# Optimization experiments

Measured on AMD Instinct MI355X. Metric: run time of the kernel, lower is better.

Reference implementation:

```python
import jax, jax.numpy as jnp
import numpy as np

D_STATE = 16; D_MODEL = 256; N_HEADS = 8; N_LAYERS = 4; D_REL = 64
HEALTH = 0
WORLD = (1024.0, 1024.0)
B, T, N = 32, 512, 8
ACTION_DIM = 12


def setup_inputs() -> dict:
    key = jax.random.key(0)
    ks = iter(jax.random.split(key, 48))
    s = 0.02
    def w(shape):
        return jax.random.normal(next(ks), shape, jnp.float32) * s
    inp = dict(
        state=jax.random.normal(next(ks), (B, T, N, D_STATE), jnp.float32),
        pos=jax.random.uniform(next(ks), (B, T, N, 2), jnp.float32),
        vel=jax.random.normal(next(ks), (B, T, N, 2), jnp.float32),
        team_ids=jax.random.randint(next(ks), (B, T, N), 0, 2, jnp.int32),
        alive=jax.random.randint(next(ks), (B, T, N), 0, 2, jnp.int32).astype(bool),
        dead=jnp.zeros((D_STATE,), jnp.float32),
        enc_W1=w((D_STATE, D_MODEL)), enc_b1=jnp.zeros((D_MODEL,), jnp.float32),
        enc_W2=w((D_MODEL, D_MODEL)), enc_b2=jnp.zeros((D_MODEL,), jnp.float32),
        team_emb=w((2, D_MODEL)), ship_emb=w((8, D_MODEL)),
        trunk_W1=w((6, D_REL)), trunk_b1=jnp.zeros((D_REL,), jnp.float32),
        trunk_W2=w((D_REL, D_REL)), trunk_b2=jnp.zeros((D_REL,), jnp.float32),
        adapt_W=w((N_LAYERS, D_REL, N_HEADS)), adapt_b=jnp.zeros((N_LAYERS, N_HEADS), jnp.float32),
        norm_w=jnp.ones((N_LAYERS, D_MODEL), jnp.float32),
        Wq=w((N_LAYERS, D_MODEL, D_MODEL)), bq=jnp.zeros((N_LAYERS, D_MODEL), jnp.float32),
        Wk=w((N_LAYERS, D_MODEL, D_MODEL)), bk=jnp.zeros((N_LAYERS, D_MODEL), jnp.float32),
        Wv=w((N_LAYERS, D_MODEL, D_MODEL)), bv=jnp.zeros((N_LAYERS, D_MODEL), jnp.float32),
        Wo=w((N_LAYERS, D_MODEL, D_MODEL)), bo=jnp.zeros((N_LAYERS, D_MODEL), jnp.float32),
        head_W=w((D_MODEL, ACTION_DIM)), head_b=jnp.zeros((ACTION_DIM,), jnp.float32),
    )
    return inp


def _rms(x, g, eps=1e-6):
    return x * jax.lax.rsqrt(jnp.mean(x * x, axis=-1, keepdims=True) + eps) * g


def reference(state, pos, vel, team_ids, alive, dead,
              enc_W1, enc_b1, enc_W2, enc_b2, team_emb, ship_emb,
              trunk_W1, trunk_b1, trunk_W2, trunk_b2, adapt_W, adapt_b,
              norm_w, Wq, bq, Wk, bk, Wv, bv, Wo, bo, head_W, head_b):
    ws = jnp.asarray(WORLD, state.dtype)
    # replace dead entities' state with learned 'dead' vector
    state = jnp.where(alive[..., None], state, dead)
    # state encoder (MLP)
    h = jax.nn.silu(state @ enc_W1 + enc_b1) @ enc_W2 + enc_b2
    # special embeddings
    h = h + team_emb[team_ids] + ship_emb[jnp.arange(N)]  # ship_emb broadcasts over B,T
    # relational trunk: pairwise toroidal geometry features [B,T,N,N,6]
    p = pos * ws
    rel = p[:, :, :, None, :] - p[:, :, None, :, :]
    rel = rel - jnp.round(rel / ws) * ws  # toroidal wrap
    relv = vel[:, :, :, None, :] - vel[:, :, None, :, :]
    dn = jnp.sqrt(jnp.sum(rel * rel, axis=-1) + 1e-8) / ws[0]
    feats = jnp.concatenate([rel / ws, relv, dn[..., None], 1.0 / (1.0 + dn[..., None])], axis=-1)
    trunk = jax.nn.silu(feats @ trunk_W1 + trunk_b1) @ trunk_W2 + trunk_b2  # [B,T,N,N,D_REL]
    dh = D_MODEL // N_HEADS
    scale = dh ** -0.5
    kmask = alive[:, :, None, None, :]  # mask keys
    x = h
    for i in range(N_LAYERS):
        nx = _rms(x, norm_w[i])
        # adapter: per-layer relational bias [B,T,H,N,N]
        bias = jnp.transpose(trunk @ adapt_W[i] + adapt_b[i], (0, 1, 4, 2, 3))
        q = (nx @ Wq[i] + bq[i]).reshape(B, T, N, N_HEADS, dh)
        k = (nx @ Wk[i] + bk[i]).reshape(B, T, N, N_HEADS, dh)
        v = (nx @ Wv[i] + bv[i]).reshape(B, T, N, N_HEADS, dh)
        sc = jnp.einsum('btihd,btjhd->bthij', q, k) * scale + bias
        sc = jnp.where(kmask, sc, -1e9)
        a = jax.nn.softmax(sc, axis=-1)
        o = jnp.einsum('bthij,btjhd->btihd', a, v).reshape(B, T, N, D_MODEL)
        x = x + o @ Wo[i] + bo[i]
    action_logits = x @ head_W + head_b  # [B,T,N,12]
    return action_logits
```

## Files before the change

### kernel.cpp

```cpp
#include <hip/hip_runtime.h>
#include <cstdint>

#define DEV __device__ __forceinline__

typedef __attribute__((ext_vector_type(8))) short short8;
typedef __attribute__((ext_vector_type(4))) float floatx4;
typedef unsigned short u16;

DEV u16 f2bf(float f) {
    unsigned u = __float_as_uint(f);
    return (u16)((u + 0x7fffu + ((u >> 16) & 1u)) >> 16);
}
DEV void unpack2(unsigned u, float& a, float& b) {
    a = __uint_as_float(u << 16);
    b = __uint_as_float(u & 0xffff0000u);
}
DEV void unpack8u(uint4 u, float* f) {
    unpack2(u.x, f[0], f[1]); unpack2(u.y, f[2], f[3]);
    unpack2(u.z, f[4], f[5]); unpack2(u.w, f[6], f[7]);
}
DEV unsigned pack2f(float a, float b) { return (unsigned)f2bf(a) | ((unsigned)f2bf(b) << 16); }
DEV uint4 pack8f(const float* f) {
    uint4 u;
    u.x = pack2f(f[0], f[1]); u.y = pack2f(f[2], f[3]);
    u.z = pack2f(f[4], f[5]); u.w = pack2f(f[6], f[7]);
    return u;
}
DEV float sigm(float x) { return 1.0f / (1.0f + __expf(-x)); }

#define NAG 8
#define DM 256
#define NL 4
#define AD 12
#define TPB 4
#define MROWS 32
#define NBLK 4096

#define OFF_E1   0
#define OFF_E2   8192
#define OFF_QKVO 73728
#define OFF_TW2  1122304
#define OFF_ADW  1126400
#define WS_TOTAL 1128448
#define WS_BYTES (WS_TOTAL * 2)

#define L_R1    0
#define L_R1B   18432
#define L_R2    36864
#define L_RED   53760
#define L_SPOS  54272
#define L_SVEL  54528
#define L_ALV   54784
#define L_TEAM  54912
#define SMEM_BYTES 55040

enum { I_STATE=0, I_POS, I_VEL, I_TEAM, I_ALIVE, I_DEAD, I_EW1, I_EB1, I_EW2, I_EB2,
       I_TEMB, I_SEMB, I_TW1, I_TB1, I_TW2, I_TB2, I_ADW, I_ADB, I_NORMW,
       I_WQ, I_BQ, I_WK, I_BK, I_WV, I_BV, I_WO, I_BO, I_HW, I_HB, N_IN };

struct Args { const void* in[N_IN]; float* out; };

__global__ __launch_bounds__(256) void prep_kernel(Args a, u16* ws)
{
    int e = blockIdx.x * 256 + threadIdx.x;
    int mat = blockIdx.y;
    int size, offs, N, Kreal;
    const float* src;
    if (mat == 0)      { size = 8192;  offs = OFF_E1;  N = 256; Kreal = 16;  src = (const float*)a.in[I_EW1]; }
    else if (mat == 1) { size = 65536; offs = OFF_E2;  N = 256; Kreal = 256; src = (const float*)a.in[I_EW2]; }
    else if (mat < 18) {
        int q = mat - 2, l = q >> 2, m = q & 3;
        int wi = (m == 0) ? I_WQ : (m == 1) ? I_WK : (m == 2) ? I_WV : I_WO;
        size = 65536; offs = OFF_QKVO + q * 65536; N = 256; Kreal = 256;
        src = (const float*)a.in[wi] + l * 65536;
    }
    else if (mat == 18) { size = 4096; offs = OFF_TW2; N = 64; Kreal = 64; src = (const float*)a.in[I_TW2]; }
    else                { size = 2048; offs = OFF_ADW; N = 32; Kreal = 64; src = (const float*)a.in[I_ADW]; }
    if (e >= size) return;
    int ksblk = N * 32;
    int ks = e / ksblk, rem = e % ksblk;
    int n = rem >> 5, quad = (rem >> 3) & 3, j = rem & 7;
    int k = ks * 32 + quad * 8 + j;
    float v = 0.0f;
    if (k < Kreal) {
        if (mat == 19) v = src[((n >> 3) * 64 + k) * 8 + (n & 7)];
        else           v = src[k * N + n];
    }
    ws[offs + e] = f2bf(v);
}

DEV short8 ld_u4(const u16* p) {
    union { uint4 u; short8 s; } c;
    c.u = *(const uint4*)p;
    return c.s;
}
DEV short8 ld_afrag(const u16* A, int stride, int row0, int kofs, int l15, int quad) {
    return ld_u4(A + (row0 + l15) * stride + kofs + quad * 8);
}
DEV short8 ld_bws(const u16* w, int ksblk, int ks, int col, int l15, int quad) {
    return ld_u4(w + ks * ksblk + (col + l15) * 32 + quad * 8);
}
DEV short8 ld_bf32(const float* W, int N, int Kreal, int ks, int col, int l15, int quad) {
    short8 r;
    #pragma unroll
    for (int j = 0; j < 8; j++) {
        int k = ks * 32 + quad * 8 + j;
        float v = (k < Kreal) ? W[k * N + col + l15] : 0.0f;
        r[j] = (short)f2bf(v);
    }
    return r;
}

template<bool UW>
DEV void gemm32(const u16* A, const u16* wsW, const float* Wf,
                int Kb, int Kreal, int colw, int l15, int quad, floatx4 acc[2][4]) {
    for (int ks = 0; ks < Kb; ks++) {
        short8 af0 = ld_afrag(A, 264, 0,  ks * 32, l15, quad);
        short8 af1 = ld_afrag(A, 264, 16, ks * 32, l15, quad);
        short8 bf[4];
        #pragma unroll
        for (int nj = 0; nj < 4; nj++)
            bf[nj] = UW ? ld_bws(wsW, 8192, ks, colw + nj * 16, l15, quad)
                        : ld_bf32(Wf, 256, Kreal, ks, colw + nj * 16, l15, quad);
        #pragma unroll
        for (int nj = 0; nj < 4; nj++) {
            acc[0][nj] = __builtin_amdgcn_mfma_f32_16x16x32_bf16(af0, bf[nj], acc[0][nj], 0, 0, 0);
            acc[1][nj] = __builtin_amdgcn_mfma_f32_16x16x32_bf16(af1, bf[nj], acc[1][nj], 0, 0, 0);
        }
    }
}

template<bool UW>
__global__ __launch_bounds__(256, 2) void yemong_mfma(Args a, const u16* ws)
{
    extern __shared__ char smem[];
    u16* sR1   = (u16*)(smem + L_R1);
    u16* sR1b  = (u16*)(smem + L_R1B);
    u16* sR2   = (u16*)(smem + L_R2);
    float* sred = (float*)(smem + L_RED);
    float* spos = (float*)(smem + L_SPOS);
    float* svel = (float*)(smem + L_SVEL);
    int* salive = (int*)(smem + L_ALV);
    int* steam  = (int*)(smem + L_TEAM);

    const int t = threadIdx.x;
    const int bid = blockIdx.x;
    const int lane = t & 63, wv = t >> 6;
    const int l15 = lane & 15, quad = lane >> 4;
    const int colw = wv * 64;

    float xr[2][4][4];
    float bias_f[4][8];
    const int tok = t >> 6, hh = (t >> 3) & 7, ii = t & 7;

    unsigned mp = 0;
    const unsigned* au = (const unsigned*)a.in[I_ALIVE];
    #pragma unroll
    for (int i = 0; i < 16; i++) mp |= au[i];
    const bool abyte = (mp > 1u);
    auto aliveAt = [&](int r) -> int {
        int gi = bid * MROWS + r;
        return abyte ? (int)((const unsigned char*)a.in[I_ALIVE])[gi]
                     : ((const int*)a.in[I_ALIVE])[gi];
    };

    if (t < MROWS) {
        salive[t] = aliveAt(t) ? 1 : 0;
        steam[t]  = ((const int*)a.in[I_TEAM])[bid * MROWS + t];
    }
    if (t >= 64 && t < 128) {
        int idx = t - 64, n = idx >> 1, d = idx & 1;
        spos[n * 2 + d] = ((const float*)a.in[I_POS])[(bid * MROWS + n) * 2 + d] * 1024.0f;
        svel[n * 2 + d] = ((const float*)a.in[I_VEL])[(bid * MROWS + n) * 2 + d];
    }
    {
        const float* gs = (const float*)a.in[I_STATE];
        const float* gd = (const float*)a.in[I_DEAD];
        #pragma unroll
        for (int it = 0; it < 4; it++) {
            int idx = t + 256 * it;
            int r = idx >> 5, kk = idx & 31;
            float v = 0.0f;
            if (kk < 16) v = aliveAt(r) ? gs[(bid * MROWS + r) * 16 + kk] : gd[kk];
            sR2[r * 264 + kk] = f2bf(v);
        }
    }
    __syncthreads();

    {
        floatx4 acc[2][4] = {};
        gemm32<UW>(sR2, ws + OFF_E1, (const float*)a.in[I_EW1], 1, 16, colw, l15, quad, acc);
        __syncthreads();
        const float* b1 = (const float*)a.in[I_EB1];
        #pragma unroll
        for (int nj = 0; nj < 4; nj++) {
            int c = colw + nj * 16 + l15;
            float bb = b1[c];
            #pragma unroll
            for (int mi = 0; mi < 2; mi++)
                #pragma unroll
                for (int r = 0; r < 4; r++) {
                    int row = mi * 16 + quad * 4 + r;
                    float v = acc[mi][nj][r] + bb;
                    sR2[row * 264 + c] = f2bf(v * sigm(v));
                }
        }
    }
    __syncthreads();

    {
        floatx4 acc[2][4] = {};
        gemm32<UW>(sR2, ws + OFF_E2, (const float*)a.in[I_EW2], 8, 256, colw, l15, quad, acc);
        const float* b2 = (const float*)a.in[I_EB2];
        const float* te = (const float*)a.in[I_TEMB];
        const float* se = (const float*)a.in[I_SEMB];
        #pragma unroll
        for (int nj = 0; nj < 4; nj++) {
            int c = colw + nj * 16 + l15;
            float bb = b2[c];
            #pragma unroll
            for (int mi = 0; mi < 2; mi++)
                #pragma unroll
                for (int r = 0; r < 4; r++) {
                    int row = mi * 16 + quad * 4 + r;
                    xr[mi][nj][r] = acc[mi][nj][r] + bb + te[steam[row] * 256 + c] + se[(row & 7) * 256 + c];
                }
        }
    }
    __syncthreads();

    {
        int ri = tok * 8 + ii, rj = tok * 8 + (t & 7);
        int pi = tok * 8 + ((t >> 3) & 7), pj = tok * 8 + (t & 7);
        float rx = spos[pi * 2 + 0] - spos[pj * 2 + 0];
        float ry = spos[pi * 2 + 1] - spos[pj * 2 + 1];
        rx -= rintf(rx * (1.0f / 1024.0f)) * 1024.0f;
        ry -= rintf(ry * (1.0f / 1024.0f)) * 1024.0f;
        float vx = svel[pi * 2 + 0] - svel[pj * 2 + 0];
        float vy = svel[pi * 2 + 1] - svel[pj * 2 + 1];
        float dn = sqrtf(rx * rx + ry * ry + 1e-8f) * (1.0f / 1024.0f);
        float f0 = rx * (1.0f / 1024.0f), f1 = ry * (1.0f / 1024.0f);
        float f4 = dn, f5 = 1.0f / (1.0f + dn);
        const float* W1 = (const float*)a.in[I_TW1];
        const float* B1 = (const float*)a.in[I_TB1];
        #pragma unroll
        for (int r = 0; r < 64; r += 2) {
            float v0 = B1[r], v1 = B1[r + 1];
            v0 = fmaf(f0, W1[r],       v0); v1 = fmaf(f0, W1[r + 1],       v1);
            v0 = fmaf(f1, W1[64 + r],  v0); v1 = fmaf(f1, W1[64 + r + 1],  v1);
            v0 = fmaf(vx, W1[128 + r], v0); v1 = fmaf(vx, W1[128 + r + 1], v1);
            v0 = fmaf(vy, W1[192 + r], v0); v1 = fmaf(vy, W1[192 + r + 1], v1);
            v0 = fmaf(f4, W1[256 + r], v0); v1 = fmaf(f4, W1[256 + r + 1], v1);
            v0 = fmaf(f5, W1[320 + r], v0); v1 = fmaf(f5, W1[320 + r + 1], v1);
            *(unsigned*)&sR1[t * 72 + r] = pack2f(v0 * sigm(v0), v1 * sigm(v1));
        }
        (void)ri; (void)rj;
    }
    __syncthreads();

    {
        short8 taf[4][2];
        #pragma unroll
        for (int mi = 0; mi < 4; mi++)
            #pragma unroll
            for (int ks = 0; ks < 2; ks++)
                taf[mi][ks] = ld_afrag(sR1, 72, colw + mi * 16, ks * 32, l15, quad);
        floatx4 tacc[4][4] = {};
        #pragma unroll
        for (int ks = 0; ks < 2; ks++) {
            short8 bf[4];
            #pragma unroll
            for (int nj = 0; nj < 4; nj++)
                bf[nj] = UW ? ld_bws(ws + OFF_TW2, 2048, ks, nj * 16, l15, quad)
                            : ld_bf32((const float*)a.in[I_TW2], 64, 64, ks, nj * 16, l15, quad);
            #pragma unroll
            for (int mi = 0; mi < 4; mi++)
                #pragma unroll
                for (int nj = 0; nj < 4; nj++)
                    tacc[mi][nj] = __builtin_amdgcn_mfma_f32_16x16x32_bf16(taf[mi][ks], bf[nj], tacc[mi][nj], 0, 0, 0);
        }
        const float* B2 = (const float*)a.in[I_TB2];
        #pragma unroll
        for (int nj = 0; nj < 4; nj++) {
            int c = nj * 16 + l15;
            float bb = B2[c];
            #pragma unroll
            for (int mi = 0; mi < 4; mi++)
                #pragma unroll
                for (int r = 0; r < 4; r++) {
                    int row = colw + mi * 16 + quad * 4 + r;
                    sR1[row * 72 + c] = f2bf(tacc[mi][nj][r] + bb);
                }
        }
    }
    __syncthreads();

    {
        floatx4 tacc[4][2] = {};
        #pragma unroll
        for (int ks = 0; ks < 2; ks++) {
            short8 bf[2];
            #pragma unroll
            for (int nj = 0; nj < 2; nj++) {
                if (UW) bf[nj] = ld_bws(ws + OFF_ADW, 1024, ks, nj * 16, l15, quad);
                else {
                    const float* adw = (const float*)a.in[I_ADW];
                    int n = nj * 16 + l15;
                    #pragma unroll
                    for (int j = 0; j < 8; j++) {
                        int k = ks * 32 + quad * 8 + j;
                        bf[nj][j] = (short)f2bf(k < 64 ? adw[((n >> 3) * 64 + k) * 8 + (n & 7)] : 0.0f);
                    }
                }
            }
            #pragma unroll
            for (int mi = 0; mi < 4; mi++) {
                short8 af = ld_afrag(sR1, 72, colw + mi * 16, ks * 32, l15, quad);
                #pragma unroll
                for (int nj = 0; nj < 2; nj++)
                    tacc[mi][nj] = __builtin_amdgcn_mfma_f32_16x16x32_bf16(af, bf[nj], tacc[mi][nj], 0, 0, 0);
            }
        }
        const float* adb = (const float*)a.in[I_ADB];
        #pragma unroll
        for (int nj = 0; nj < 2; nj++) {
            int n = nj * 16 + l15;
            float bb = adb[n];
            #pragma unroll
            for (int mi = 0; mi < 4; mi++)
                #pragma unroll
                for (int r = 0; r < 4; r++) {
                    int pl = mi * 16 + quad * 4 + r;
                    sR2[((wv * 4 + (n >> 3)) * 8 + (n & 7)) * 64 + pl] = f2bf(tacc[mi][nj][r] + bb);
                }
        }
        __syncthreads();
        #pragma unroll
        for (int l = 0; l < 4; l++) {
            uint4 u = *(const uint4*)&sR2[((tok * 4 + l) * 8 + hh) * 64 + ii * 8];
            unpack8u(u, bias_f[l]);
        }
    }

    const float* normw = (const float*)a.in[I_NORMW];
    for (int l = 0; l < NL; l++) {
        float invr[8];
        {
            float ssv[8];
            #pragma unroll
            for (int mi = 0; mi < 2; mi++)
                #pragma unroll
                for (int r = 0; r < 4; r++) {
                    float s = 0.0f;
                    #pragma unroll
                    for (int nj = 0; nj < 4; nj++) { float v = xr[mi][nj][r]; s = fmaf(v, v, s); }
                    ssv[mi * 4 + r] = s;
                }
            #pragma unroll
            for (int m = 1; m < 16; m <<= 1)
                #pragma unroll
                for (int k2 = 0; k2 < 8; k2++) ssv[k2] += __shfl_xor(ssv[k2], m);
            if (l15 == 0) {
                #pragma unroll
                for (int mi = 0; mi < 2; mi++)
                    #pragma unroll
                    for (int r = 0; r < 4; r++)
                        sred[(mi * 16 + quad * 4 + r) * 4 + wv] = ssv[mi * 4 + r];
            }
            __syncthreads();
            #pragma unroll
            for (int mi = 0; mi < 2; mi++)
                #pragma unroll
                for (int r = 0; r < 4; r++) {
                    int row = mi * 16 + quad * 4 + r;
                    float s = sred[row * 4 + 0] + sred[row * 4 + 1] + sred[row * 4 + 2] + sred[row * 4 + 3];
                    invr[mi * 4 + r] = rsqrtf(s * (1.0f / 256.0f) + 1e-6f);
                }
        }
        {
            float nwv[4];
            #pragma unroll
            for (int nj = 0; nj < 4; nj++) nwv[nj] = normw[l * 256 + colw + nj * 16 + l15];
            #pragma unroll
            for (int nj = 0; nj < 4; nj++) {
                int c = colw + nj * 16 + l15;
                #pragma unroll
                for (int mi = 0; mi < 2; mi++)
                    #pragma unroll
                    for (int r = 0; r < 4; r++)
                        sR2[(mi * 16 + quad * 4 + r) * 264 + c] = f2bf(xr[mi][nj][r] * invr[mi * 4 + r] * nwv[nj]);
            }
        }
        __syncthreads();

        {
            floatx4 acc[3][2][4] = {};
            const u16* wq = ws + OFF_QKVO + (l * 4 + 0) * 65536;
            const u16* wk = ws + OFF_QKVO + (l * 4 + 1) * 65536;
            const u16* wvv = ws + OFF_QKVO + (l * 4 + 2) * 65536;
            const float* fq = (const float*)a.in[I_WQ] + l * 65536;
            const float* fk = (const float*)a.in[I_WK] + l * 65536;
            const float* fv = (const float*)a.in[I_WV] + l * 65536;
            #pragma unroll 2
            for (int ks = 0; ks < 8; ks++) {
                short8 af0 = ld_afrag(sR2, 264, 0,  ks * 32, l15, quad);
                short8 af1 = ld_afrag(sR2, 264, 16, ks * 32, l15, quad);
                short8 bq[4], bk[4], bv[4];
                #pragma unroll
                for (int nj = 0; nj < 4; nj++) {
                    int c = colw + nj * 16;
                    bq[nj] = UW ? ld_bws(wq,  8192, ks, c, l15, quad) : ld_bf32(fq, 256, 256, ks, c, l15, quad);
                    bk[nj] = UW ? ld_bws(wk,  8192, ks, c, l15, quad) : ld_bf32(fk, 256, 256, ks, c, l15, quad);
                    bv[nj] = UW ? ld_bws(wvv, 8192, ks, c, l15, quad) : ld_bf32(fv, 256, 256, ks, c, l15, quad);
                }
                #pragma unroll
                for (int nj = 0; nj < 4; nj++) {
                    acc[0][0][nj] = __builtin_amdgcn_mfma_f32_16x16x32_bf16(af0, bq[nj], acc[0][0][nj], 0, 0, 0);
                    acc[0][1][nj] = __builtin_amdgcn_mfma_f32_16x16x32_bf16(af1, bq[nj], acc[0][1][nj], 0, 0, 0);
                    acc[1][0][nj] = __builtin_amdgcn_mfma_f32_16x16x32_bf16(af0, bk[nj], acc[1][0][nj], 0, 0, 0);
                    acc[1][1][nj] = __builtin_amdgcn_mfma_f32_16x16x32_bf16(af1, bk[nj], acc[1][1][nj], 0, 0, 0);
                    acc[2][0][nj] = __builtin_amdgcn_mfma_f32_16x16x32_bf16(af0, bv[nj], acc[2][0][nj], 0, 0, 0);
                    acc[2][1][nj] = __builtin_amdgcn_mfma_f32_16x16x32_bf16(af1, bv[nj], acc[2][1][nj], 0, 0, 0);
                }
            }
            const float* bqf = (const float*)a.in[I_BQ] + l * 256;
            const float* bkf = (const float*)a.in[I_BK] + l * 256;
            #pragma unroll
            for (int nj = 0; nj < 4; nj++) {
                int c = colw + nj * 16 + l15;
                float b0 = bqf[c], b1 = bkf[c];
                #pragma unroll
                for (int mi = 0; mi < 2; mi++)
                    #pragma unroll
                    for (int r = 0; r < 4; r++) {
                        int row = mi * 16 + quad * 4 + r;
                        sR1 [row * 264 + c] = f2bf(acc[0][mi][nj][r] + b0);
                        sR1b[row * 264 + c] = f2bf(acc[1][mi][nj][r] + b1);
                    }
            }
            __syncthreads();
            const float* bvf = (const float*)a.in[I_BV] + l * 256;
            #pragma unroll
            for (int nj = 0; nj < 4; nj++) {
                int c = colw + nj * 16 + l15;
                float b2v = bvf[c];
                #pragma unroll
                for (int mi = 0; mi < 2; mi++)
                    #pragma unroll
                    for (int r = 0; r < 4; r++)
                        sR2[(mi * 16 + quad * 4 + r) * 264 + c] = f2bf(acc[2][mi][nj][r] + b2v);
            }
        }

        float p[8];
        {
            int rq = tok * 8 + ii;
            float qv[32];
            #pragma unroll
            for (int g = 0; g < 4; g++) {
                uint4 u = *(const uint4*)&sR1[rq * 264 + hh * 32 + g * 8];
                unpack8u(u, &qv[g * 8]);
            }
            float sc[8];
            #pragma unroll
            for (int j = 0; j < 8; j++) {
                int rk = tok * 8 + j;
                float dot = 0.0f;
                #pragma unroll
                for (int g = 0; g < 4; g++) {
                    uint4 u = *(const uint4*)&sR1b[rk * 264 + hh * 32 + g * 8];
                    float kf[8];
                    unpack8u(u, kf);
                    #pragma unroll
                    for (int e2 = 0; e2 < 8; e2++) dot = fmaf(qv[g * 8 + e2], kf[e2], dot);
                }
                sc[j] = salive[tok * 8 + j] ? fmaf(dot, 0.17677669529663689f, bias_f[l][j]) : -1000000000.0f;
            }
            float mx = sc[0];
            #pragma unroll
            for (int j = 1; j < 8; j++) mx = fmaxf(mx, sc[j]);
            float s = 0.0f;
            #pragma unroll
            for (int j = 0; j < 8; j++) { p[j] = __expf(sc[j] - mx); s += p[j]; }
            float inv = 1.0f / s;
            #pragma unroll
            for (int j = 0; j < 8; j++) p[j] *= inv;
        }
        __syncthreads();

        {
            float o[32];
            #pragma unroll
            for (int cc = 0; cc < 32; cc++) o[cc] = 0.0f;
            #pragma unroll
            for (int j = 0; j < 8; j++) {
                float pj = p[j];
                int rv = tok * 8 + j;
                #pragma unroll
                for (int g = 0; g < 4; g++) {
                    uint4 u = *(const uint4*)&sR2[rv * 264 + hh * 32 + g * 8];
                    float vf[8];
                    unpack8u(u, vf);
                    #pragma unroll
                    for (int e2 = 0; e2 < 8; e2++) o[g * 8 + e2] = fmaf(pj, vf[e2], o[g * 8 + e2]);
                }
            }
            int rq = tok * 8 + ii;
            #pragma unroll
            for (int g = 0; g < 4; g++)
                *(uint4*)&sR1[rq * 264 + hh * 32 + g * 8] = pack8f(&o[g * 8]);
        }
        __syncthreads();

        {
            floatx4 acc[2][4] = {};
            gemm32<UW>(sR1, ws + OFF_QKVO + (l * 4 + 3) * 65536, (const float*)a.in[I_WO] + l * 65536,
                       8, 256, colw, l15, quad, acc);
            const float* bo = (const float*)a.in[I_BO] + l * 256;
            #pragma unroll
            for (int nj = 0; nj < 4; nj++) {
                float bb = bo[colw + nj * 16 + l15];
                #pragma unroll
                for (int mi = 0; mi < 2; mi++)
                    #pragma unroll
                    for (int r = 0; r < 4; r++)
                        xr[mi][nj][r] += acc[mi][nj][r] + bb;
            }
        }
        __syncthreads();
    }

    {
        float* xf = (float*)sR1;
        #pragma unroll
        for (int nj = 0; nj < 4; nj++) {
            int c = colw + nj * 16 + l15;
            #pragma unroll
            for (int mi = 0; mi < 2; mi++)
                #pragma unroll
                for (int r = 0; r < 4; r++)
                    xf[(mi * 16 + quad * 4 + r) * 264 + c] = xr[mi][nj][r];
        }
        __syncthreads();
        int row = t >> 3, pp = t & 7;
        const float* HW = (const float*)a.in[I_HW];
        float ah[12];
        #pragma unroll
        for (int c = 0; c < 12; c++) ah[c] = 0.0f;
        for (int kk = pp * 32; kk < pp * 32 + 32; kk++) {
            float xv = xf[row * 264 + kk];
            #pragma unroll
            for (int c = 0; c < 12; c++) ah[c] = fmaf(xv, HW[kk * 12 + c], ah[c]);
        }
        #pragma unroll
        for (int c = 0; c < 12; c++) {
            ah[c] += __shfl_xor(ah[c], 1);
            ah[c] += __shfl_xor(ah[c], 2);
            ah[c] += __shfl_xor(ah[c], 4);
        }
        if (pp == 0) {
            const float* hb = (const float*)a.in[I_HB];
            #pragma unroll
            for (int c = 0; c < 12; c++)
                a.out[(bid * MROWS + row) * AD + c] = ah[c] + hb[c];
        }
    }
}

extern "C" void kernel_launch(void* const* d_in, const int* in_sizes, int n_in,
                              void* d_out, int out_size, void* d_ws, size_t ws_size,
                              hipStream_t stream) {
    (void)in_sizes; (void)n_in; (void)out_size;
    Args a;
    for (int i = 0; i < N_IN; i++) a.in[i] = d_in[i];
    a.out = (float*)d_out;
    u16* ws16 = (u16*)d_ws;
    const bool use_ws = (ws_size >= (size_t)WS_BYTES) && (d_ws != nullptr);
    if (use_ws) {
        hipLaunchKernelGGL(prep_kernel, dim3(256, 20), dim3(256), 0, stream, a, ws16);
        hipFuncSetAttribute((const void*)yemong_mfma<true>, hipFuncAttributeMaxDynamicSharedMemorySize, SMEM_BYTES);
        hipLaunchKernelGGL((yemong_mfma<true>), dim3(NBLK), dim3(256), SMEM_BYTES, stream, a, ws16);
    } else {
        hipFuncSetAttribute((const void*)yemong_mfma<false>, hipFuncAttributeMaxDynamicSharedMemorySize, SMEM_BYTES);
        hipLaunchKernelGGL((yemong_mfma<false>), dim3(NBLK), dim3(256), SMEM_BYTES, stream, a, ws16);
    }
}
```

Measured before the change: 1.093 ms.

## Move per-layer attention onto MFMA with register-held bias and smaller LDS

Attention scores and P·V now run on 16x16x32 bf16 MFMA per head pair of tokens, replacing the scalar per-thread dot products. The softmax is done with cross-lane shuffles. Relational bias and the alive mask are kept in packed registers instead of LDS or float arrays. The fused QKV GEMM is split into three sequential gemm32 calls to cut register pressure. The trunk buffer is XOR-swizzled, which together shrinks shared memory so launch bounds can allow 3 blocks per CU. The trade-off is that half of each MFMA tile is wasted through masking, and the V fragments are gathered element by element.

```diff
diff --git a/kernel.cpp b/kernel.cpp
--- a/kernel.cpp
+++ b/kernel.cpp
@@ -6,33 +6,23 @@
 typedef __attribute__((ext_vector_type(8))) short short8;
 typedef __attribute__((ext_vector_type(4))) float floatx4;
 typedef unsigned short u16;
+typedef unsigned int u32;
 
 DEV u16 f2bf(float f) {
     unsigned u = __float_as_uint(f);
     return (u16)((u + 0x7fffu + ((u >> 16) & 1u)) >> 16);
 }
-DEV void unpack2(unsigned u, float& a, float& b) {
+DEV void unpack2(u32 u, float& a, float& b) {
     a = __uint_as_float(u << 16);
     b = __uint_as_float(u & 0xffff0000u);
 }
-DEV void unpack8u(uint4 u, float* f) {
-    unpack2(u.x, f[0], f[1]); unpack2(u.y, f[2], f[3]);
-    unpack2(u.z, f[4], f[5]); unpack2(u.w, f[6], f[7]);
-}
-DEV unsigned pack2f(float a, float b) { return (unsigned)f2bf(a) | ((unsigned)f2bf(b) << 16); }
-DEV uint4 pack8f(const float* f) {
-    uint4 u;
-    u.x = pack2f(f[0], f[1]); u.y = pack2f(f[2], f[3]);
-    u.z = pack2f(f[4], f[5]); u.w = pack2f(f[6], f[7]);
-    return u;
-}
+DEV u32 pack2f(float a, float b) { return (u32)f2bf(a) | ((u32)f2bf(b) << 16); }
 DEV float sigm(float x) { return 1.0f / (1.0f + __expf(-x)); }
 
 #define NAG 8
 #define DM 256
 #define NL 4
 #define AD 12
-#define TPB 4
 #define MROWS 32
 #define NBLK 4096
 
@@ -45,14 +35,13 @@
 #define WS_BYTES (WS_TOTAL * 2)
 
 #define L_R1    0
-#define L_R1B   18432
-#define L_R2    36864
-#define L_RED   53760
-#define L_SPOS  54272
-#define L_SVEL  54528
-#define L_ALV   54784
-#define L_TEAM  54912
-#define SMEM_BYTES 55040
+#define L_R2    33792
+#define L_RED   50688
+#define L_SPOS  51200
+#define L_SVEL  51456
+#define SMEM_BYTES 51712
+
+#define TRK(row, col) ((row) * 64 + ((((col) >> 3) ^ ((row) & 7)) << 3) + ((col) & 7))
 
 enum { I_STATE=0, I_POS, I_VEL, I_TEAM, I_ALIVE, I_DEAD, I_EW1, I_EB1, I_EW2, I_EB2,
        I_TEMB, I_SEMB, I_TW1, I_TB1, I_TW2, I_TB2, I_ADW, I_ADB, I_NORMW,
@@ -131,27 +120,25 @@
 }
 
 template<bool UW>
-__global__ __launch_bounds__(256, 2) void yemong_mfma(Args a, const u16* ws)
+__global__ __launch_bounds__(256, 3) void yemong_mfma(Args a, const u16* ws)
 {
     extern __shared__ char smem[];
     u16* sR1   = (u16*)(smem + L_R1);
-    u16* sR1b  = (u16*)(smem + L_R1B);
+    u16* skb   = (u16*)(smem + L_R1 + 16896);
     u16* sR2   = (u16*)(smem + L_R2);
     float* sred = (float*)(smem + L_RED);
     float* spos = (float*)(smem + L_SPOS);
     float* svel = (float*)(smem + L_SVEL);
-    int* salive = (int*)(smem + L_ALV);
-    int* steam  = (int*)(smem + L_TEAM);
-
-    const int t = threadIdx.x;
-    const int bid = blockIdx.x;
-    const int lane = t & 63, wv = t >> 6;
+
+    const int t = threadIdx.x, bid = blockIdx.x;
+    const int lane = t & 63, w = t >> 6;
     const int l15 = lane & 15, quad = lane >> 4;
-    const int colw = wv * 64;
+    const int colw = w * 64;
+    const int p = w >> 1, h0 = (w & 1) * 4;
 
     float xr[2][4][4];
-    float bias_f[4][8];
-    const int tok = t >> 6, hh = (t >> 3) & 7, ii = t & 7;
+    u32 br[NL][4][2];
+    u32 amask;
 
     unsigned mp = 0;
     const unsigned* au = (const unsigned*)a.in[I_ALIVE];
@@ -164,14 +151,16 @@
                      : ((const int*)a.in[I_ALIVE])[gi];
     };
 
-    if (t < MROWS) {
-        salive[t] = aliveAt(t) ? 1 : 0;
-        steam[t]  = ((const int*)a.in[I_TEAM])[bid * MROWS + t];
-    }
-    if (t >= 64 && t < 128) {
-        int idx = t - 64, n = idx >> 1, d = idx & 1;
+    if (t < 64) {
+        int n = t >> 1, d = t & 1;
         spos[n * 2 + d] = ((const float*)a.in[I_POS])[(bid * MROWS + n) * 2 + d] * 1024.0f;
         svel[n * 2 + d] = ((const float*)a.in[I_VEL])[(bid * MROWS + n) * 2 + d];
+    }
+    {
+        int tk = 2 * p + (quad >> 1);
+        amask = 0;
+        #pragma unroll
+        for (int j = 0; j < 8; j++) amask |= (aliveAt(tk * 8 + j) ? 1u : 0u) << j;
     }
     {
         const float* gs = (const float*)a.in[I_STATE];
@@ -200,9 +189,8 @@
             for (int mi = 0; mi < 2; mi++)
                 #pragma unroll
                 for (int r = 0; r < 4; r++) {
-                    int row = mi * 16 + quad * 4 + r;
                     float v = acc[mi][nj][r] + bb;
-                    sR2[row * 264 + c] = f2bf(v * sigm(v));
+                    sR2[(mi * 16 + quad * 4 + r) * 264 + c] = f2bf(v * sigm(v));
                 }
         }
     }
@@ -214,6 +202,13 @@
         const float* b2 = (const float*)a.in[I_EB2];
         const float* te = (const float*)a.in[I_TEMB];
         const float* se = (const float*)a.in[I_SEMB];
+        const int* gteam = (const int*)a.in[I_TEAM];
+        int team8[8];
+        #pragma unroll
+        for (int mi = 0; mi < 2; mi++)
+            #pragma unroll
+            for (int r = 0; r < 4; r++)
+                team8[mi * 4 + r] = gteam[bid * MROWS + mi * 16 + quad * 4 + r];
         #pragma unroll
         for (int nj = 0; nj < 4; nj++) {
             int c = colw + nj * 16 + l15;
@@ -223,15 +218,14 @@
                 #pragma unroll
                 for (int r = 0; r < 4; r++) {
                     int row = mi * 16 + quad * 4 + r;
-                    xr[mi][nj][r] = acc[mi][nj][r] + bb + te[steam[row] * 256 + c] + se[(row & 7) * 256 + c];
-                }
-        }
-    }
-    __syncthreads();
-
-    {
-        int ri = tok * 8 + ii, rj = tok * 8 + (t & 7);
-        int pi = tok * 8 + ((t >> 3) & 7), pj = tok * 8 + (t & 7);
+                    xr[mi][nj][r] = acc[mi][nj][r] + bb + te[team8[mi * 4 + r] * 256 + c] + se[(row & 7) * 256 + c];
+                }
+        }
+    }
+
+    {
+        int tokp = t >> 6;
+        int pi = tokp * 8 + ((t >> 3) & 7), pj = tokp * 8 + (t & 7);
         float rx = spos[pi * 2 + 0] - spos[pj * 2 + 0];
         float ry = spos[pi * 2 + 1] - spos[pj * 2 + 1];
         rx -= rintf(rx * (1.0f / 1024.0f)) * 1024.0f;
@@ -239,22 +233,25 @@
         float vx = svel[pi * 2 + 0] - svel[pj * 2 + 0];
         float vy = svel[pi * 2 + 1] - svel[pj * 2 + 1];
         float dn = sqrtf(rx * rx + ry * ry + 1e-8f) * (1.0f / 1024.0f);
-        float f0 = rx * (1.0f / 1024.0f), f1 = ry * (1.0f / 1024.0f);
-        float f4 = dn, f5 = 1.0f / (1.0f + dn);
+        float f[6] = {rx * (1.0f / 1024.0f), ry * (1.0f / 1024.0f), vx, vy, dn, 1.0f / (1.0f + dn)};
         const float* W1 = (const float*)a.in[I_TW1];
         const float* B1 = (const float*)a.in[I_TB1];
         #pragma unroll
-        for (int r = 0; r < 64; r += 2) {
-            float v0 = B1[r], v1 = B1[r + 1];
-            v0 = fmaf(f0, W1[r],       v0); v1 = fmaf(f0, W1[r + 1],       v1);
-            v0 = fmaf(f1, W1[64 + r],  v0); v1 = fmaf(f1, W1[64 + r + 1],  v1);
-            v0 = fmaf(vx, W1[128 + r], v0); v1 = fmaf(vx, W1[128 + r + 1], v1);
-            v0 = fmaf(vy, W1[192 + r], v0); v1 = fmaf(vy, W1[192 + r + 1], v1);
-            v0 = fmaf(f4, W1[256 + r], v0); v1 = fmaf(f4, W1[256 + r + 1], v1);
-            v0 = fmaf(f5, W1[320 + r], v0); v1 = fmaf(f5, W1[320 + r + 1], v1);
-            *(unsigned*)&sR1[t * 72 + r] = pack2f(v0 * sigm(v0), v1 * sigm(v1));
-        }
-        (void)ri; (void)rj;
+        for (int g = 0; g < 8; g++) {
+            float v[8];
+            #pragma unroll
+            for (int e = 0; e < 8; e++) v[e] = B1[g * 8 + e];
+            #pragma unroll
+            for (int kk = 0; kk < 6; kk++)
+                #pragma unroll
+                for (int e = 0; e < 8; e++) v[e] = fmaf(f[kk], W1[kk * 64 + g * 8 + e], v[e]);
+            #pragma unroll
+            for (int e = 0; e < 8; e++) v[e] = v[e] * sigm(v[e]);
+            uint4 pk;
+            pk.x = pack2f(v[0], v[1]); pk.y = pack2f(v[2], v[3]);
+            pk.z = pack2f(v[4], v[5]); pk.w = pack2f(v[6], v[7]);
+            *(uint4*)&sR1[t * 64 + ((g ^ (t & 7)) << 3)] = pk;
+        }
     }
     __syncthreads();
 
@@ -263,8 +260,10 @@
         #pragma unroll
         for (int mi = 0; mi < 4; mi++)
             #pragma unroll
-            for (int ks = 0; ks < 2; ks++)
-                taf[mi][ks] = ld_afrag(sR1, 72, colw + mi * 16, ks * 32, l15, quad);
+            for (int ks = 0; ks < 2; ks++) {
+                int R = colw + mi * 16 + l15;
+                taf[mi][ks] = ld_u4(&sR1[R * 64 + (((ks * 4 + quad) ^ (R & 7)) << 3)]);
+            }
         floatx4 tacc[4][4] = {};
         #pragma unroll
         for (int ks = 0; ks < 2; ks++) {
@@ -289,7 +288,7 @@
                 #pragma unroll
                 for (int r = 0; r < 4; r++) {
                     int row = colw + mi * 16 + quad * 4 + r;
-                    sR1[row * 72 + c] = f2bf(tacc[mi][nj][r] + bb);
+                    sR1[TRK(row, c)] = f2bf(tacc[mi][nj][r] + bb);
                 }
         }
     }
@@ -315,7 +314,8 @@
             }
             #pragma unroll
             for (int mi = 0; mi < 4; mi++) {
-                short8 af = ld_afrag(sR1, 72, colw + mi * 16, ks * 32, l15, quad);
+                int R = colw + mi * 16 + l15;
+                short8 af = ld_u4(&sR1[R * 64 + (((ks * 4 + quad) ^ (R & 7)) << 3)]);
                 #pragma unroll
                 for (int nj = 0; nj < 2; nj++)
                     tacc[mi][nj] = __builtin_amdgcn_mfma_f32_16x16x32_bf16(af, bf[nj], tacc[mi][nj], 0, 0, 0);
@@ -331,18 +331,25 @@
                 #pragma unroll
                 for (int r = 0; r < 4; r++) {
                     int pl = mi * 16 + quad * 4 + r;
-                    sR2[((wv * 4 + (n >> 3)) * 8 + (n & 7)) * 64 + pl] = f2bf(tacc[mi][nj][r] + bb);
-                }
-        }
-        __syncthreads();
-        #pragma unroll
-        for (int l = 0; l < 4; l++) {
-            uint4 u = *(const uint4*)&sR2[((tok * 4 + l) * 8 + hh) * 64 + ii * 8];
-            unpack8u(u, bias_f[l]);
-        }
-    }
+                    sR2[((w * 4 + (n >> 3)) * 8 + (n & 7)) * 64 + pl] = f2bf(tacc[mi][nj][r] + bb);
+                }
+        }
+        __syncthreads();
+        int tk = 2 * p + (quad >> 1);
+        #pragma unroll
+        for (int l = 0; l < NL; l++)
+            #pragma unroll
+            for (int u = 0; u < 4; u++) {
+                int base = ((tk * 4 + l) * 8 + (h0 + u)) * 64 + (l15 & 7) * 8 + (quad & 1) * 4;
+                const u32* bp = (const u32*)&sR2[base];
+                br[l][u][0] = bp[0];
+                br[l][u][1] = bp[1];
+            }
+    }
+    __syncthreads();
 
     const float* normw = (const float*)a.in[I_NORMW];
+    const bool qvalid = ((quad >> 1) == (l15 >> 3));
     for (int l = 0; l < NL; l++) {
         float invr[8];
         {
@@ -365,7 +372,7 @@
                 for (int mi = 0; mi < 2; mi++)
                     #pragma unroll
                     for (int r = 0; r < 4; r++)
-                        sred[(mi * 16 + quad * 4 + r) * 4 + wv] = ssv[mi * 4 + r];
+                        sred[(mi * 16 + quad * 4 + r) * 4 + w] = ssv[mi * 4 + r];
             }
             __syncthreads();
             #pragma unroll
@@ -378,137 +385,118 @@
                 }
         }
         {
-            float nwv[4];
-            #pragma unroll
-            for (int nj = 0; nj < 4; nj++) nwv[nj] = normw[l * 256 + colw + nj * 16 + l15];
             #pragma unroll
             for (int nj = 0; nj < 4; nj++) {
                 int c = colw + nj * 16 + l15;
+                float nwv = normw[l * 256 + c];
                 #pragma unroll
                 for (int mi = 0; mi < 2; mi++)
                     #pragma unroll
                     for (int r = 0; r < 4; r++)
-                        sR2[(mi * 16 + quad * 4 + r) * 264 + c] = f2bf(xr[mi][nj][r] * invr[mi * 4 + r] * nwv[nj]);
+                        sR2[(mi * 16 + quad * 4 + r) * 264 + c] = f2bf(xr[mi][nj][r] * invr[mi * 4 + r] * nwv);
             }
         }
         __syncthreads();
 
         {
-            floatx4 acc[3][2][4] = {};
-            const u16* wq = ws + OFF_QKVO + (l * 4 + 0) * 65536;
-            const u16* wk = ws + OFF_QKVO + (l * 4 + 1) * 65536;
-            const u16* wvv = ws + OFF_QKVO + (l * 4 + 2) * 65536;
-            const float* fq = (const float*)a.in[I_WQ] + l * 65536;
-            const float* fk = (const float*)a.in[I_WK] + l * 65536;
-            const float* fv = (const float*)a.in[I_WV] + l * 65536;
-            #pragma unroll 2
-            for (int ks = 0; ks < 8; ks++) {
-                short8 af0 = ld_afrag(sR2, 264, 0,  ks * 32, l15, quad);
-                short8 af1 = ld_afrag(sR2, 264, 16, ks * 32, l15, quad);
-                short8 bq[4], bk[4], bv[4];
-                #pragma unroll
-                for (int nj = 0; nj < 4; nj++) {
-                    int c = colw + nj * 16;
-                    bq[nj] = UW ? ld_bws(wq,  8192, ks, c, l15, quad) : ld_bf32(fq, 256, 256, ks, c, l15, quad);
-                    bk[nj] = UW ? ld_bws(wk,  8192, ks, c, l15, quad) : ld_bf32(fk, 256, 256, ks, c, l15, quad);
-                    bv[nj] = UW ? ld_bws(wvv, 8192, ks, c, l15, quad) : ld_bf32(fv, 256, 256, ks, c, l15, quad);
-                }
-                #pragma unroll
-                for (int nj = 0; nj < 4; nj++) {
-                    acc[0][0][nj] = __builtin_amdgcn_mfma_f32_16x16x32_bf16(af0, bq[nj], acc[0][0][nj], 0, 0, 0);
-                    acc[0][1][nj] = __builtin_amdgcn_mfma_f32_16x16x32_bf16(af1, bq[nj], acc[0][1][nj], 0, 0, 0);
-                    acc[1][0][nj] = __builtin_amdgcn_mfma_f32_16x16x32_bf16(af0, bk[nj], acc[1][0][nj], 0, 0, 0);
-                    acc[1][1][nj] = __builtin_amdgcn_mfma_f32_16x16x32_bf16(af1, bk[nj], acc[1][1][nj], 0, 0, 0);
-                    acc[2][0][nj] = __builtin_amdgcn_mfma_f32_16x16x32_bf16(af0, bv[nj], acc[2][0][nj], 0, 0, 0);
-                    acc[2][1][nj] = __builtin_amdgcn_mfma_f32_16x16x32_bf16(af1, bv[nj], acc[2][1][nj], 0, 0, 0);
-                }
-            }
-            const float* bqf = (const float*)a.in[I_BQ] + l * 256;
-            const float* bkf = (const float*)a.in[I_BK] + l * 256;
+            floatx4 acc[2][4] = {};
+            gemm32<UW>(sR2, ws + OFF_QKVO + (l * 4 + 0) * 65536, (const float*)a.in[I_WQ] + l * 65536, 8, 256, colw, l15, quad, acc);
+            const float* bq = (const float*)a.in[I_BQ] + l * 256;
             #pragma unroll
             for (int nj = 0; nj < 4; nj++) {
                 int c = colw + nj * 16 + l15;
-                float b0 = bqf[c], b1 = bkf[c];
+                float bb = bq[c];
                 #pragma unroll
                 for (int mi = 0; mi < 2; mi++)
                     #pragma unroll
-                    for (int r = 0; r < 4; r++) {
-                        int row = mi * 16 + quad * 4 + r;
-                        sR1 [row * 264 + c] = f2bf(acc[0][mi][nj][r] + b0);
-                        sR1b[row * 264 + c] = f2bf(acc[1][mi][nj][r] + b1);
-                    }
-            }
-            __syncthreads();
-            const float* bvf = (const float*)a.in[I_BV] + l * 256;
+                    for (int r = 0; r < 4; r++)
+                        sR1[(mi * 16 + quad * 4 + r) * 264 + c] = f2bf((acc[mi][nj][r] + bb) * 0.17677669529663689f);
+            }
+        }
+        {
+            floatx4 acc[2][4] = {};
+            gemm32<UW>(sR2, ws + OFF_QKVO + (l * 4 + 1) * 65536, (const float*)a.in[I_WK] + l * 65536, 8, 256, colw, l15, quad, acc);
+            const float* bk = (const float*)a.in[I_BK] + l * 256;
             #pragma unroll
             for (int nj = 0; nj < 4; nj++) {
                 int c = colw + nj * 16 + l15;
-                float b2v = bvf[c];
+                float bb = bk[c];
                 #pragma unroll
                 for (int mi = 0; mi < 2; mi++)
                     #pragma unroll
                     for (int r = 0; r < 4; r++)
-                        sR2[(mi * 16 + quad * 4 + r) * 264 + c] = f2bf(acc[2][mi][nj][r] + b2v);
-            }
-        }
-
-        float p[8];
+                        skb[(mi * 16 + quad * 4 + r) * 264 + c] = f2bf(acc[mi][nj][r] + bb);
+            }
+        }
         {
-            int rq = tok * 8 + ii;
-            float qv[32];
-            #pragma unroll
-            for (int g = 0; g < 4; g++) {
-                uint4 u = *(const uint4*)&sR1[rq * 264 + hh * 32 + g * 8];
-                unpack8u(u, &qv[g * 8]);
-            }
-            float sc[8];
-            #pragma unroll
-            for (int j = 0; j < 8; j++) {
-                int rk = tok * 8 + j;
-                float dot = 0.0f;
-                #pragma unroll
-                for (int g = 0; g < 4; g++) {
-                    uint4 u = *(const uint4*)&sR1b[rk * 264 + hh * 32 + g * 8];
-                    float kf[8];
-                    unpack8u(u, kf);
-                    #pragma unroll
-                    for (int e2 = 0; e2 < 8; e2++) dot = fmaf(qv[g * 8 + e2], kf[e2], dot);
-                }
-                sc[j] = salive[tok * 8 + j] ? fmaf(dot, 0.17677669529663689f, bias_f[l][j]) : -1000000000.0f;
-            }
-            float mx = sc[0];
-            #pragma unroll
-            for (int j = 1; j < 8; j++) mx = fmaxf(mx, sc[j]);
-            float s = 0.0f;
-            #pragma unroll
-            for (int j = 0; j < 8; j++) { p[j] = __expf(sc[j] - mx); s += p[j]; }
-            float inv = 1.0f / s;
-            #pragma unroll
-            for (int j = 0; j < 8; j++) p[j] *= inv;
-        }
-        __syncthreads();
-
-        {
-            float o[32];
-            #pragma unroll
-            for (int cc = 0; cc < 32; cc++) o[cc] = 0.0f;
-            #pragma unroll
-            for (int j = 0; j < 8; j++) {
-                float pj = p[j];
-                int rv = tok * 8 + j;
-                #pragma unroll
-                for (int g = 0; g < 4; g++) {
-                    uint4 u = *(const uint4*)&sR2[rv * 264 + hh * 32 + g * 8];
-                    float vf[8];
-                    unpack8u(u, vf);
-                    #pragma unroll
-                    for (int e2 = 0; e2 < 8; e2++) o[g * 8 + e2] = fmaf(pj, vf[e2], o[g * 8 + e2]);
-                }
-            }
-            int rq = tok * 8 + ii;
-            #pragma unroll
-            for (int g = 0; g < 4; g++)
-                *(uint4*)&sR1[rq * 264 + hh * 32 + g * 8] = pack8f(&o[g * 8]);
+            floatx4 acc[2][4] = {};
+            gemm32<UW>(sR2, ws + OFF_QKVO + (l * 4 + 2) * 65536, (const float*)a.in[I_WV] + l * 65536, 8, 256, colw, l15, quad, acc);
+            __syncthreads();
+            const float* bv = (const float*)a.in[I_BV] + l * 256;
+            #pragma unroll
+            for (int nj = 0; nj < 4; nj++) {
+                int c = colw + nj * 16 + l15;
+                float bb = bv[c];
+                #pragma unroll
+                for (int mi = 0; mi < 2; mi++)
+                    #pragma unroll
+                    for (int r = 0; r < 4; r++)
+                        sR2[(mi * 16 + quad * 4 + r) * 264 + c] = f2bf(acc[mi][nj][r] + bb);
+            }
+        }
+        __syncthreads();
+
+        #pragma unroll
+        for (int u = 0; u < 4; u++) {
+            int h = h0 + u;
+            short8 kf = ld_u4(&skb[(p * 16 + l15) * 264 + h * 32 + quad * 8]);
+            short8 qf = ld_u4(&sR1[(p * 16 + l15) * 264 + h * 32 + quad * 8]);
+            floatx4 zero = {};
+            floatx4 st = __builtin_amdgcn_mfma_f32_16x16x32_bf16(kf, qf, zero, 0, 0, 0);
+            float bb[4];
+            unpack2(br[l][u][0], bb[0], bb[1]);
+            unpack2(br[l][u][1], bb[2], bb[3]);
+            float s[4];
+            #pragma unroll
+            for (int r = 0; r < 4; r++) {
+                int jl = (quad & 1) * 4 + r;
+                bool alv = (amask >> jl) & 1;
+                s[r] = qvalid ? (alv ? st[r] + bb[r] : -1.0e9f) : -2.0e9f;
+            }
+            float mx = fmaxf(fmaxf(s[0], s[1]), fmaxf(s[2], s[3]));
+            mx = fmaxf(mx, __shfl_xor(mx, 16));
+            mx = fmaxf(mx, __shfl_xor(mx, 32));
+            float e[4], sm = 0.0f;
+            #pragma unroll
+            for (int r = 0; r < 4; r++) { e[r] = __expf(s[r] - mx); sm += e[r]; }
+            sm += __shfl_xor(sm, 16);
+            sm += __shfl_xor(sm, 32);
+            float inv = 1.0f / sm;
+            u32 u01 = pack2f(e[0] * inv, e[1] * inv);
+            u32 u23 = pack2f(e[2] * inv, e[3] * inv);
+            int srcA = (quad * 32 + l15) & 63;
+            u32 a0 = (u32)__shfl((int)u01, srcA);
+            u32 a1 = (u32)__shfl((int)u23, srcA);
+            u32 a2 = (u32)__shfl((int)u01, (srcA + 16) & 63);
+            u32 a3 = (u32)__shfl((int)u23, (srcA + 16) & 63);
+            if (quad >= 2) { a0 = 0; a1 = 0; a2 = 0; a3 = 0; }
+            union { u32 uu[4]; short8 ss; } cv;
+            cv.uu[0] = a0; cv.uu[1] = a1; cv.uu[2] = a2; cv.uu[3] = a3;
+            short8 paf = cv.ss;
+            #pragma unroll
+            for (int nt = 0; nt < 2; nt++) {
+                short8 vf;
+                #pragma unroll
+                for (int jj = 0; jj < 8; jj++) {
+                    int kr = (quad * 8 + jj) & 15;
+                    vf[jj] = (short)sR2[(p * 16 + kr) * 264 + h * 32 + nt * 16 + l15];
+                }
+                floatx4 z2 = {};
+                floatx4 o = __builtin_amdgcn_mfma_f32_16x16x32_bf16(paf, vf, z2, 0, 0, 0);
+                #pragma unroll
+                for (int r = 0; r < 4; r++)
+                    sR1[(p * 16 + quad * 4 + r) * 264 + h * 32 + nt * 16 + l15] = f2bf(o[r]);
+            }
         }
         __syncthreads();
 
```

Result: slower. 1.299 ms (+18.8%).
